# Performance work log

Hardware: AMD Instinct MI355X
Metric: run time of the kernel (lower is better)

## Reference

```python
import jax, jax.numpy as jnp
import numpy as np

EMBED_DIM = 1024
NUM_HEADS = 16
HEAD_DIM = EMBED_DIM // NUM_HEADS


def setup_inputs() -> dict:
    key = jax.random.key(0)
    kx, kq, kk, kv = jax.random.split(key, 4)
    x = jax.random.normal(kx, (4, 2048, EMBED_DIM), dtype=jnp.float32)
    s = 1.0 / np.sqrt(EMBED_DIM)
    # nn.Linear weight layout: [out, in]; y = x @ W.T
    w_q = jax.random.uniform(kq, (EMBED_DIM, EMBED_DIM), jnp.float32, -s, s)
    w_k = jax.random.uniform(kk, (EMBED_DIM, EMBED_DIM), jnp.float32, -s, s)
    w_v = jax.random.uniform(kv, (EMBED_DIM, EMBED_DIM), jnp.float32, -s, s)
    return {"x": x, "w_q": w_q, "w_k": w_k, "w_v": w_v}


def reference(x, w_q, w_k, w_v):
    B, S, E = x.shape
    H, D = NUM_HEADS, HEAD_DIM
    # projections (Linear without bias): x @ W.T, split into heads
    q = (x @ w_q.T).reshape(B, S, H, D).transpose(0, 2, 1, 3)  # [B,H,S,D]
    k = (x @ w_k.T).reshape(B, S, H, D).transpose(0, 2, 1, 3)  # [B,H,S,D]
    v = (x @ w_v.T).reshape(B, S, H, D).transpose(0, 2, 1, 3)  # [B,H,S,D]
    # NOTE: original scales by sqrt(embed_dim), not sqrt(head_dim)
    scores = jnp.einsum('bhqd,bhkd->bhqk', q, k) / jnp.sqrt(jnp.float32(E))
    attn = jax.nn.softmax(scores, axis=-1)
    out = jnp.einsum('bhqk,bhkd->bhqd', attn, v)
    # concat heads; original forward never applies fc_out
    return out.transpose(0, 2, 1, 3).reshape(B, S, E)
```

## Files before the change

### kernel.cpp

```cpp
#include <hip/hip_runtime.h>
#include <hip/hip_bf16.h>

typedef __hip_bfloat16 bf16;
typedef float f32x4 __attribute__((ext_vector_type(4)));
typedef short bf16x8 __attribute__((ext_vector_type(8)));
typedef short bf16x4 __attribute__((ext_vector_type(4)));
typedef unsigned u32x4 __attribute__((ext_vector_type(4)));

#define DI __device__ __forceinline__

constexpr int B_ = 4, S_ = 2048, E_ = 1024, H_ = 16, D_ = 64;
constexpr int M_ = B_ * S_;
constexpr float QSCALE = 0.03125f * 1.4426950408889634f;

DI unsigned short bfbits(float f) {
  __hip_bfloat16 h = __float2bfloat16(f);
  return *reinterpret_cast<unsigned short*>(&h);
}

DI unsigned cvt_pk_bf16(float lo, float hi) {
  unsigned r;
  asm("v_cvt_pk_bf16_f32 %0, %1, %2" : "=v"(r) : "v"(lo), "v"(hi));
  return r;
}

DI void gload_lds16(const bf16* g, bf16* l) {
  __builtin_amdgcn_global_load_lds((const __attribute__((address_space(1))) void*)g,
                                   (__attribute__((address_space(3))) void*)l, 16, 0, 0);
}

__global__ __launch_bounds__(256) void cast_all(const float* __restrict__ x,
                                                const float* __restrict__ wq,
                                                const float* __restrict__ wk,
                                                const float* __restrict__ wv,
                                                ushort* __restrict__ xb,
                                                ushort* __restrict__ wqb,
                                                ushort* __restrict__ wkb,
                                                ushort* __restrict__ wvb) {
  int id = blockIdx.x * 256 + threadIdx.x;
  const float* src; ushort* dst; int i;
  if (id < 2097152)      { src = x;  dst = xb;  i = id; }
  else if (id < 2359296) { src = wq; dst = wqb; i = id - 2097152; }
  else if (id < 2621440) { src = wk; dst = wkb; i = id - 2359296; }
  else                   { src = wv; dst = wvb; i = id - 2621440; }
  float4 v = reinterpret_cast<const float4*>(src)[i];
  ushort4 o;
  o.x = bfbits(v.x); o.y = bfbits(v.y); o.z = bfbits(v.z); o.w = bfbits(v.w);
  reinterpret_cast<ushort4*>(dst)[i] = o;
}

__global__ __launch_bounds__(256) void gemm_qkv_fused(const bf16* __restrict__ A,
                                                      const bf16* __restrict__ Wq,
                                                      const bf16* __restrict__ Wk,
                                                      const bf16* __restrict__ Wv,
                                                      bf16* __restrict__ Qh,
                                                      bf16* __restrict__ Kh,
                                                      bf16* __restrict__ Vth) {
  constexpr int BM = 128, BN = 128, BK = 32, NK = E_ / BK;
  __shared__ __align__(16) bf16 As[2][BM * BK];
  __shared__ __align__(16) bf16 Bs[2][BN * BK];
  const int t = threadIdx.x, l = t & 63, w = t >> 6;
  const int wm = w >> 1, wn = w & 1;

  const int bid = blockIdx.x;
  const int xcd = bid & 7, jq = bid >> 3;
  const int m0 = (xcd * 8 + (jq & 7)) * BM;
  const int ntile = jq >> 3;
  const int sec = ntile >> 3;
  const int n0 = (ntile & 7) * BN;
  const bf16* W = sec == 0 ? Wq : (sec == 1 ? Wk : Wv);

  f32x4 acc[4][4] = {};

  auto stage = [&](int buf, int kt) {
#pragma unroll
    for (int i = 0; i < 2; ++i) {
      int t2 = i * 256 + t;
      int r = t2 >> 2, sl = t2 & 3;
      int g = sl ^ ((r >> 1) & 3);
      gload_lds16(A + (size_t)(m0 + r) * E_ + kt * BK + g * 8,
                  &As[buf][(size_t)(i * 256 + w * 64) * 8]);
      gload_lds16(W + (size_t)(n0 + r) * E_ + kt * BK + g * 8,
                  &Bs[buf][(size_t)(i * 256 + w * 64) * 8]);
    }
  };

  auto tile = [&](int buf) {
    bf16x8 af[4], bfr[4];
#pragma unroll
    for (int i = 0; i < 4; ++i) {
      int ra = wm * 64 + i * 16 + (l & 15);
      int sla = (l >> 4) ^ ((ra >> 1) & 3);
      af[i] = *reinterpret_cast<const bf16x8*>(&As[buf][(ra * 4 + sla) * 8]);
      int rb = wn * 64 + i * 16 + (l & 15);
      int slb = (l >> 4) ^ ((rb >> 1) & 3);
      bfr[i] = *reinterpret_cast<const bf16x8*>(&Bs[buf][(rb * 4 + slb) * 8]);
    }
#pragma unroll
    for (int i = 0; i < 4; ++i)
#pragma unroll
      for (int j = 0; j < 4; ++j)
        acc[i][j] = __builtin_amdgcn_mfma_f32_16x16x32_bf16(af[i], bfr[j], acc[i][j], 0, 0, 0);
  };

  stage(0, 0);
  for (int kt = 0; kt < NK; kt += 2) {
    __syncthreads();
    if (kt + 1 < NK) stage(1, kt + 1);
    tile(0);
    __syncthreads();
    if (kt + 2 < NK) stage(0, kt + 2);
    tile(1);
  }

  const float oscale = (sec == 0) ? QSCALE : 1.0f;
  bf16* dst = sec == 0 ? Qh : (sec == 1 ? Kh : Vth);
#pragma unroll
  for (int i = 0; i < 4; ++i)
#pragma unroll
    for (int j = 0; j < 4; ++j)
#pragma unroll
      for (int jj = 0; jj < 4; ++jj) {
        int mr = m0 + wm * 64 + i * 16 + (l >> 4) * 4 + jj;
        int nc = n0 + wn * 64 + j * 16 + (l & 15);
        int b = mr >> 11, s = mr & 2047, h = nc >> 6, d = nc & 63;
        size_t idx;
        if (sec == 2) idx = ((size_t)(b * H_ + h) * D_ + d) * S_ + s;
        else          idx = ((size_t)(b * H_ + h) * S_ + s) * D_ + d;
        dst[idx] = __float2bfloat16(acc[i][j][jj] * oscale);
      }
}

__global__ __launch_bounds__(256) void attn_kernel(const bf16* __restrict__ Q,
                                                   const bf16* __restrict__ K,
                                                   const bf16* __restrict__ Vt,
                                                   float* __restrict__ out) {
  constexpr int KT = 64, NT = S_ / KT;
  __shared__ __align__(16) bf16 Ks[2][KT * D_];
  __shared__ __align__(16) bf16 Vs[2][D_ * KT];

  const int t = threadIdx.x, l = t & 63, w = t >> 6;
  const int hi = l >> 4, r15 = l & 15;
  const int p = blockIdx.x;
  const int lg = (p & 7) * 256 + (p >> 3);
  const int qblk = lg & 31, h = (lg >> 5) & 15, b = lg >> 9;
  const int q0 = qblk * 64 + w * 16;
  const size_t bh = (size_t)(b * H_ + h);
  const bf16* Qb = Q + bh * S_ * D_;
  const bf16* Kb = K + bh * S_ * D_;
  const bf16* Vb = Vt + bh * D_ * S_;

  bf16x8 aq[2];
#pragma unroll
  for (int c = 0; c < 2; ++c)
    aq[c] = *reinterpret_cast<const bf16x8*>(Qb + (size_t)(q0 + r15) * D_ + c * 32 + hi * 8);

  int koff[2][4], voff[2][4][2];
#pragma unroll
  for (int c = 0; c < 2; ++c)
#pragma unroll
    for (int nt = 0; nt < 4; ++nt) {
      int r = nt * 16 + r15;
      koff[c][nt] = (r * D_ + ((4 * c + hi) ^ (r & 7)) * 8) * 2;
      int d = nt * 16 + r15;
#pragma unroll
      for (int hf = 0; hf < 2; ++hf) {
        int blk = 4 * c + 2 * hf + (hi >> 1);
        voff[c][nt][hf] = (d * KT + ((blk ^ (d & 7)) * 8) + 4 * (hi & 1)) * 2;
      }
    }

  f32x4 o_acc[4] = {};
  float lsum = 0.f;

  auto stage = [&](int buf, int kt) {
    const bf16* Kt_ = Kb + (size_t)kt * KT * D_;
    const bf16* Vt_ = Vb + kt * KT;
#pragma unroll
    for (int i = 0; i < 2; ++i) {
      int idx = i * 256 + t;
      int rr = idx >> 3, s = idx & 7;
      int g = s ^ (rr & 7);
      gload_lds16(Kt_ + rr * D_ + g * 8, &Ks[buf][(i * 256 + w * 64) * 8]);
      gload_lds16(Vt_ + (size_t)rr * S_ + g * 8, &Vs[buf][(i * 256 + w * 64) * 8]);
    }
  };

  auto tile = [&](int buf) {
    const char* kbase = (const char*)Ks[buf];
    const char* vbase = (const char*)Vs[buf];
    f32x4 sc[4] = {};
#pragma unroll
    for (int c = 0; c < 2; ++c)
#pragma unroll
      for (int nt = 0; nt < 4; ++nt) {
        bf16x8 bk = *reinterpret_cast<const bf16x8*>(kbase + koff[c][nt]);
        sc[nt] = __builtin_amdgcn_mfma_f32_16x16x32_bf16(bk, aq[c], sc[nt], 0, 0, 0);
      }
    u32x4 pa[2];
#pragma unroll
    for (int nt = 0; nt < 4; ++nt) {
      float pf0 = __builtin_amdgcn_exp2f(sc[nt][0]);
      float pf1 = __builtin_amdgcn_exp2f(sc[nt][1]);
      float pf2 = __builtin_amdgcn_exp2f(sc[nt][2]);
      float pf3 = __builtin_amdgcn_exp2f(sc[nt][3]);
      lsum += (pf0 + pf1) + (pf2 + pf3);
      pa[nt >> 1][(nt & 1) * 2 + 0] = cvt_pk_bf16(pf0, pf1);
      pa[nt >> 1][(nt & 1) * 2 + 1] = cvt_pk_bf16(pf2, pf3);
    }
#pragma unroll
    for (int c = 0; c < 2; ++c) {
      bf16x8 ap = __builtin_bit_cast(bf16x8, pa[c]);
#pragma unroll
      for (int nt = 0; nt < 4; ++nt) {
        bf16x4 v0 = *reinterpret_cast<const bf16x4*>(vbase + voff[c][nt][0]);
        bf16x4 v1 = *reinterpret_cast<const bf16x4*>(vbase + voff[c][nt][1]);
        bf16x8 bv;
#pragma unroll
        for (int e = 0; e < 4; ++e) { bv[e] = v0[e]; bv[e + 4] = v1[e]; }
        o_acc[nt] = __builtin_amdgcn_mfma_f32_16x16x32_bf16(ap, bv, o_acc[nt], 0, 0, 0);
      }
    }
  };

  stage(0, 0);
  for (int kt = 0; kt < NT; kt += 2) {
    __syncthreads();
    if (kt + 1 < NT) stage(1, kt + 1);
    tile(0);
    __syncthreads();
    if (kt + 2 < NT) stage(0, kt + 2);
    tile(1);
  }

  lsum += __shfl_xor(lsum, 16);
  lsum += __shfl_xor(lsum, 32);
  float inv = 1.f / lsum;
#pragma unroll
  for (int jj = 0; jj < 4; ++jj) {
    float invj = __shfl(inv, (l & 48) + hi * 4 + jj);
    int q = q0 + hi * 4 + jj;
#pragma unroll
    for (int nt = 0; nt < 4; ++nt) {
      int d = nt * 16 + r15;
      out[((size_t)b * S_ + q) * E_ + h * D_ + d] = o_acc[nt][jj] * invj;
    }
  }
}

extern "C" void kernel_launch(void* const* d_in, const int* in_sizes, int n_in,
                              void* d_out, int out_size, void* d_ws, size_t ws_size,
                              hipStream_t stream) {
  const float* x = (const float*)d_in[0];
  const float* wq = (const float*)d_in[1];
  const float* wk = (const float*)d_in[2];
  const float* wv = (const float*)d_in[3];
  float* out = (float*)d_out;
  char* ws = (char*)d_ws;

  bf16* xb  = (bf16*)(ws + 0);
  bf16* wqb = (bf16*)(ws + 16777216);
  bf16* wkb = (bf16*)(ws + 18874368);
  bf16* wvb = (bf16*)(ws + 20971520);
  bf16* Qh  = (bf16*)(ws + 23068672);
  bf16* Kh  = (bf16*)(ws + 39845888);
  bf16* Vth = (bf16*)(ws + 56623104);

  cast_all<<<11264, 256, 0, stream>>>(x, wq, wk, wv, (ushort*)xb, (ushort*)wqb,
                                      (ushort*)wkb, (ushort*)wvb);

  gemm_qkv_fused<<<1536, 256, 0, stream>>>(xb, wqb, wkb, wvb, Qh, Kh, Vth);

  attn_kernel<<<2048, 256, 0, stream>>>(Qh, Kh, Vth, out);
}
```

Before: 278.7 us.

## Rewrite QKV GEMM with 256x256 tiles, 4-stage LDS ring and staged epilogue

```diff
diff --git a/kernel.cpp b/kernel.cpp
--- a/kernel.cpp
+++ b/kernel.cpp
@@ -49,86 +49,133 @@
   reinterpret_cast<ushort4*>(dst)[i] = o;
 }
 
-__global__ __launch_bounds__(256) void gemm_qkv_fused(const bf16* __restrict__ A,
-                                                      const bf16* __restrict__ Wq,
-                                                      const bf16* __restrict__ Wk,
-                                                      const bf16* __restrict__ Wv,
-                                                      bf16* __restrict__ Qh,
-                                                      bf16* __restrict__ Kh,
-                                                      bf16* __restrict__ Vth) {
-  constexpr int BM = 128, BN = 128, BK = 32, NK = E_ / BK;
-  __shared__ __align__(16) bf16 As[2][BM * BK];
-  __shared__ __align__(16) bf16 Bs[2][BN * BK];
+__global__ __launch_bounds__(512, 2) void gemm_qkv_8ph(const bf16* __restrict__ A,
+                                                       const bf16* __restrict__ W,
+                                                       bf16* __restrict__ Qh,
+                                                       bf16* __restrict__ Kh,
+                                                       bf16* __restrict__ Vth) {
+  constexpr int NG = E_ / 32;
+  __shared__ __align__(16) bf16 lds[65536];
   const int t = threadIdx.x, l = t & 63, w = t >> 6;
-  const int wm = w >> 1, wn = w & 1;
+  const int hi = l >> 4, r15 = l & 15;
+  const int wm = w >> 2, wn = w & 3;
 
   const int bid = blockIdx.x;
-  const int xcd = bid & 7, jq = bid >> 3;
-  const int m0 = (xcd * 8 + (jq & 7)) * BM;
-  const int ntile = jq >> 3;
-  const int sec = ntile >> 3;
-  const int n0 = (ntile & 7) * BN;
-  const bf16* W = sec == 0 ? Wq : (sec == 1 ? Wk : Wv);
-
-  f32x4 acc[4][4] = {};
-
-  auto stage = [&](int buf, int kt) {
-#pragma unroll
-    for (int i = 0; i < 2; ++i) {
-      int t2 = i * 256 + t;
-      int r = t2 >> 2, sl = t2 & 3;
-      int g = sl ^ ((r >> 1) & 3);
-      gload_lds16(A + (size_t)(m0 + r) * E_ + kt * BK + g * 8,
-                  &As[buf][(size_t)(i * 256 + w * 64) * 8]);
-      gload_lds16(W + (size_t)(n0 + r) * E_ + kt * BK + g * 8,
-                  &Bs[buf][(size_t)(i * 256 + w * 64) * 8]);
+  const int swz = (bid & 7) * 48 + (bid >> 3);
+  const int mt = swz / 12, nt = swz - mt * 12;
+  const int m0 = mt * 256, n0 = nt * 256;
+
+  f32x4 acc[8][4] = {};
+
+  auto stageM = [&](int g, int kind) {
+    const bf16* src = (kind == 0) ? A + (size_t)m0 * E_ : W + (size_t)n0 * E_;
+    bf16* base = lds + (size_t)(g & 3) * 16384 + kind * 8192 + (w * 64) * 8;
+#pragma unroll
+    for (int i2 = 0; i2 < 2; ++i2) {
+      int gr = i2 * 512 + t;
+      int row = gr >> 2, slot = gr & 3;
+      int ch = slot ^ (row & 3);
+      gload_lds16(src + (size_t)row * E_ + g * 32 + ch * 8, base + i2 * 4096);
     }
   };
 
-  auto tile = [&](int buf) {
-    bf16x8 af[4], bfr[4];
-#pragma unroll
-    for (int i = 0; i < 4; ++i) {
-      int ra = wm * 64 + i * 16 + (l & 15);
-      int sla = (l >> 4) ^ ((ra >> 1) & 3);
-      af[i] = *reinterpret_cast<const bf16x8*>(&As[buf][(ra * 4 + sla) * 8]);
-      int rb = wn * 64 + i * 16 + (l & 15);
-      int slb = (l >> 4) ^ ((rb >> 1) & 3);
-      bfr[i] = *reinterpret_cast<const bf16x8*>(&Bs[buf][(rb * 4 + slb) * 8]);
-    }
-#pragma unroll
-    for (int i = 0; i < 4; ++i)
-#pragma unroll
-      for (int j = 0; j < 4; ++j)
-        acc[i][j] = __builtin_amdgcn_mfma_f32_16x16x32_bf16(af[i], bfr[j], acc[i][j], 0, 0, 0);
-  };
-
-  stage(0, 0);
-  for (int kt = 0; kt < NK; kt += 2) {
-    __syncthreads();
-    if (kt + 1 < NK) stage(1, kt + 1);
-    tile(0);
-    __syncthreads();
-    if (kt + 2 < NK) stage(0, kt + 2);
-    tile(1);
+  stageM(0, 0); stageM(0, 1);
+  stageM(1, 0); stageM(1, 1);
+  asm volatile("s_waitcnt vmcnt(4)" ::: "memory");
+  __builtin_amdgcn_s_barrier();
+
+  for (int g = 0; g < NG; ++g) {
+    const char* sa = (const char*)(lds + (size_t)(g & 3) * 16384);
+    const char* sb = sa + 8192 * 2;
+    bf16x8 bfrag[4];
+#pragma unroll
+    for (int mg = 0; mg < 2; ++mg) {
+      bf16x8 afrag[4];
+#pragma unroll
+      for (int mm = 0; mm < 4; ++mm) {
+        int row = wm * 128 + (mg * 4 + mm) * 16 + r15;
+        afrag[mm] = *(const bf16x8*)(sa + row * 64 + ((hi ^ (row & 3)) * 16));
+      }
+      if (mg == 0) {
+#pragma unroll
+        for (int nf = 0; nf < 4; ++nf) {
+          int row = wn * 64 + nf * 16 + r15;
+          bfrag[nf] = *(const bf16x8*)(sb + row * 64 + ((hi ^ (row & 3)) * 16));
+        }
+      }
+      if (g < NG - 2) stageM(g + 2, mg);
+      __builtin_amdgcn_s_barrier();
+      asm volatile("s_waitcnt lgkmcnt(0)" ::: "memory");
+      __builtin_amdgcn_sched_barrier(0);
+      __builtin_amdgcn_s_setprio(1);
+#pragma unroll
+      for (int mm = 0; mm < 4; ++mm)
+#pragma unroll
+        for (int nf = 0; nf < 4; ++nf)
+          acc[mg * 4 + mm][nf] =
+              __builtin_amdgcn_mfma_f32_16x16x32_bf16(afrag[mm], bfrag[nf],
+                                                      acc[mg * 4 + mm][nf], 0, 0, 0);
+      __builtin_amdgcn_s_setprio(0);
+      if (mg == 1) {
+        if (g < NG - 2)       asm volatile("s_waitcnt vmcnt(4)" ::: "memory");
+        else if (g == NG - 2) asm volatile("s_waitcnt vmcnt(0)" ::: "memory");
+      }
+      __builtin_amdgcn_s_barrier();
+    }
   }
 
-  const float oscale = (sec == 0) ? QSCALE : 1.0f;
-  bf16* dst = sec == 0 ? Qh : (sec == 1 ? Kh : Vth);
-#pragma unroll
-  for (int i = 0; i < 4; ++i)
-#pragma unroll
-    for (int j = 0; j < 4; ++j)
-#pragma unroll
-      for (int jj = 0; jj < 4; ++jj) {
-        int mr = m0 + wm * 64 + i * 16 + (l >> 4) * 4 + jj;
-        int nc = n0 + wn * 64 + j * 16 + (l & 15);
-        int b = mr >> 11, s = mr & 2047, h = nc >> 6, d = nc & 63;
-        size_t idx;
-        if (sec == 2) idx = ((size_t)(b * H_ + h) * D_ + d) * S_ + s;
-        else          idx = ((size_t)(b * H_ + h) * S_ + s) * D_ + d;
-        dst[idx] = __float2bfloat16(acc[i][j][jj] * oscale);
-      }
+  const int ncol0 = n0 + wn * 64;
+  const int sec = ncol0 >> 10;
+  const int h = (ncol0 >> 6) & 15;
+  const int mrow = m0 + wm * 128;
+  const int b = mrow >> 11, sbase = mrow & 2047;
+  char* wb = (char*)lds + w * 16384;
+
+  if (sec < 2) {
+    bf16* dst = sec == 0 ? Qh : Kh;
+    const float osc = sec == 0 ? QSCALE : 1.0f;
+#pragma unroll
+    for (int mf = 0; mf < 8; ++mf)
+#pragma unroll
+      for (int nf = 0; nf < 4; ++nf)
+#pragma unroll
+        for (int jj = 0; jj < 4; ++jj) {
+          int s = mf * 16 + 4 * hi + jj;
+          int d = nf * 16 + r15;
+          *(bf16*)(wb + s * 128 + ((d * 2) ^ ((s & 7) << 4))) =
+              __float2bfloat16(acc[mf][nf][jj] * osc);
+        }
+    asm volatile("s_waitcnt lgkmcnt(0)" ::: "memory");
+    __builtin_amdgcn_sched_barrier(0);
+    bf16* obase = dst + ((size_t)(b * H_ + h) * S_ + sbase) * D_;
+#pragma unroll
+    for (int c = 0; c < 16; ++c) {
+      int s = c * 8 + (l >> 3), dch = l & 7;
+      bf16x8 v = *(const bf16x8*)(wb + s * 128 + ((dch * 16) ^ ((s & 7) << 4)));
+      *(bf16x8*)(obase + (size_t)s * D_ + dch * 8) = v;
+    }
+  } else {
+#pragma unroll
+    for (int mf = 0; mf < 8; ++mf)
+#pragma unroll
+      for (int nf = 0; nf < 4; ++nf)
+#pragma unroll
+        for (int m2 = 0; m2 < 2; ++m2) {
+          int s = mf * 16 + 4 * hi + m2 * 2;
+          int d = nf * 16 + r15;
+          unsigned u = cvt_pk_bf16(acc[mf][nf][m2 * 2], acc[mf][nf][m2 * 2 + 1]);
+          *(unsigned*)(wb + d * 256 + ((s * 2) ^ ((d & 7) << 4))) = u;
+        }
+    asm volatile("s_waitcnt lgkmcnt(0)" ::: "memory");
+    __builtin_amdgcn_sched_barrier(0);
+    const int d = l;
+    bf16* obase = Vth + ((size_t)(b * H_ + h) * D_ + d) * S_ + sbase;
+#pragma unroll
+    for (int c = 0; c < 16; ++c) {
+      bf16x8 v = *(const bf16x8*)(wb + d * 256 + ((c * 16) ^ ((d & 7) << 4)));
+      *(bf16x8*)(obase + c * 8) = v;
+    }
+  }
 }
 
 __global__ __launch_bounds__(256) void attn_kernel(const bf16* __restrict__ Q,
@@ -269,7 +316,7 @@
   cast_all<<<11264, 256, 0, stream>>>(x, wq, wk, wv, (ushort*)xb, (ushort*)wqb,
                                       (ushort*)wkb, (ushort*)wvb);
 
-  gemm_qkv_fused<<<1536, 256, 0, stream>>>(xb, wqb, wkb, wvb, Qh, Kh, Vth);
+  gemm_qkv_8ph<<<384, 512, 0, stream>>>(xb, wqb, Qh, Kh, Vth);
 
   attn_kernel<<<2048, 256, 0, stream>>>(Qh, Kh, Vth, out);
 }
```

Result: faster. 265.3 us (-4.8%).
